# Kernel tuning notes

Hardware: AMD Instinct MI355X
Metric: run time of the kernel (lower is better)

Reference implementation:

```python
import jax, jax.numpy as jnp
import numpy as np

N_USERS = 100_000
N_ITEMS = 50_000
N = N_USERS + N_ITEMS  # total nodes in the normalized UI adjacency
D = 128                # emb_size == hyper_size
NNZ = 1_500_000        # nonzeros in sparse_norm_adj (COO)
EPS = 1e-5             # torch.nn.LayerNorm default eps


def setup_inputs() -> dict:
    key = jax.random.key(0)
    k1, k2, k3, k4 = jax.random.split(key, 4)
    return {
        "ego_embeddings": jax.random.normal(k1, (N, D), dtype=jnp.float32),
        "adj_vals": jax.random.uniform(k2, (NNZ,), dtype=jnp.float32),
        "ln_gamma": jnp.ones((D,), dtype=jnp.float32),
        "ln_beta": jnp.zeros((D,), dtype=jnp.float32),
        "adj_rows": jax.random.randint(k3, (NNZ,), 0, N, dtype=jnp.int32),
        "adj_cols": jax.random.randint(k4, (NNZ,), 0, N, dtype=jnp.int32),
    }


def _layer_norm(x, gamma, beta):
    mu = jnp.mean(x, axis=-1, keepdims=True)
    var = jnp.var(x, axis=-1, keepdims=True)
    return (x - mu) * jax.lax.rsqrt(var + EPS) * gamma + beta


def reference(ego_embeddings, adj_vals, ln_gamma, ln_beta, adj_rows, adj_cols):
    # HGCNConv with act=False: adj @ (adj.T @ embs), adj sparse COO [N, N]
    # (A^T @ x)[c] = sum_{(r,c) in nnz} vals * x[r]
    h = jax.ops.segment_sum(adj_vals[:, None] * ego_embeddings[adj_rows], adj_cols, num_segments=N)
    # (A @ h)[r] = sum_{(r,c) in nnz} vals * h[c]
    h2 = jax.ops.segment_sum(adj_vals[:, None] * h[adj_cols], adj_rows, num_segments=N)
    # LayerNorm + residual (last-layer branch of LocalAwareEncoder.forward)
    out = _layer_norm(h2, ln_gamma, ln_beta) + ego_embeddings
    user_all_embeddings = out[:N_USERS]
    item_all_embeddings = out[N_USERS:]
    return user_all_embeddings, item_all_embeddings
```

## Files before the change

### kernel.cpp

```cpp
#include <hip/hip_runtime.h>

#define N_TOTAL 150000
#define DIM 128
#define NNZ_E 1500000
#define NBUCK 256
#define DPB 586
#define EPB2 2048
#define A2_BLOCKS ((NNZ_E + EPB2 - 1) / EPB2)
#define CONV_BLOCKS 9375
#define HIST_BLOCKS 512
#define MAXE 16
#define G1_BLOCKS (N_TOTAL / 8)
#define SLAB_CAP 8192

typedef unsigned long long u64;
typedef unsigned uvec16 __attribute__((ext_vector_type(16)));
typedef unsigned uvec2  __attribute__((ext_vector_type(2)));

__device__ __forceinline__ unsigned pack_bf16_bits(unsigned ua, unsigned ub) {
    ua = (ua + 0x7FFFu + ((ua >> 16) & 1u)) >> 16;
    ub = (ub + 0x7FFFu + ((ub >> 16) & 1u)) >> 16;
    return ua | (ub << 16);
}
__device__ __forceinline__ unsigned pack_bf16(float a, float b) {
    return pack_bf16_bits(__float_as_uint(a), __float_as_uint(b));
}
__device__ __forceinline__ float2 unpack_bf16(unsigned u) {
    return make_float2(__uint_as_float(u << 16), __uint_as_float(u & 0xFFFF0000u));
}
__device__ __forceinline__ float rdlane_f(float x, int l) {
    return __uint_as_float((unsigned)__builtin_amdgcn_readlane((int)__float_as_uint(x), l));
}

__device__ __forceinline__ int wave_iscan(int v, int lane) {
    #pragma unroll
    for (int o = 1; o < 64; o <<= 1) {
        int u = __shfl_up(v, o, 64);
        if (lane >= o) v += u;
    }
    return v;
}
__device__ __forceinline__ int blk_escan512(int v, int t, int* wsum) {
    int lane = t & 63, wv = t >> 6;
    int inc = wave_iscan(v, lane);
    if (lane == 63) wsum[wv] = inc;
    __syncthreads();
    if (t < 64) {
        int x = (t < 8) ? wsum[t] : 0;
        int p = wave_iscan(x, t);
        if (t < 8) wsum[t] = p - x;
    }
    __syncthreads();
    return wsum[wv] + inc - v;
}

__device__ __forceinline__ void sload_pair(uvec16 &a, uvec16 &b, const void* p) {
    asm volatile("s_load_dwordx16 %0, %2, 0x0\n\t"
                 "s_load_dwordx16 %1, %2, 0x40\n\t"
                 "s_waitcnt lgkmcnt(0)"
                 : "=&s"(a), "=&s"(b) : "s"(p) : "memory");
}
__device__ __forceinline__ void sload_be(uvec2 &r, const void* p) {
    asm volatile("s_load_dwordx2 %0, %1, 0x0\n\t"
                 "s_waitcnt lgkmcnt(0)"
                 : "=&s"(r) : "s"(p) : "memory");
}

__device__ __forceinline__ void chunk8(const uvec16 &m, int lim, int lane,
                                       const uint* __restrict__ srcBf,
                                       float &ax, float &ay, float &bx, float &by) {
    #pragma unroll
    for (int j = 0; j < 8; j++) {
        unsigned sx = (j < lim) ? (m[2 * j] & 0x3FFFFu) : 0u;
        float vv = (j < lim) ? __uint_as_float(m[2 * j + 1]) : 0.0f;
        const uint* p = srcBf + ((size_t)sx << 6);
        float2 uu = unpack_bf16(p[lane]);
        if (j & 1) { bx += vv * uu.x; by += vv * uu.y; }
        else       { ax += vv * uu.x; ay += vv * uu.y; }
    }
}

__device__ __forceinline__ void gather_row(const uint* __restrict__ srcBf,
                                           const int* __restrict__ offs,
                                           const uint2* __restrict__ edges,
                                           int row_u, int lane,
                                           float &ax, float &ay, float &bx, float &by) {
    uvec2 be;
    sload_be(be, offs + row_u);
    int beg = (int)be[0];
    int n = (int)be[1] - beg;
    const u64* ep = (const u64*)edges + beg;
    uvec16 mA, mB;
    sload_pair(mA, mB, ep);
    chunk8(mA, n < 8 ? n : 8, lane, srcBf, ax, ay, bx, by);
    if (n > 8) {
        chunk8(mB, n - 8 < 8 ? n - 8 : 8, lane, srcBf, ax, ay, bx, by);
        if (n > 16) {
            uvec16 mC, mD;
            sload_pair(mC, mD, ep + 16);
            chunk8(mC, n - 16 < 8 ? n - 16 : 8, lane, srcBf, ax, ay, bx, by);
            if (n > 24) {
                chunk8(mD, n - 24 < 8 ? n - 24 : 8, lane, srcBf, ax, ay, bx, by);
                for (int k = 32; k < n; k++) {
                    uint2 e = edges[beg + k];
                    float v = __uint_as_float(e.y);
                    float2 u = unpack_bf16(srcBf[(((size_t)e.x) << 6) + lane]);
                    ax += v * u.x; ay += v * u.y;
                }
            }
        }
    }
}

__global__ __launch_bounds__(256) void conv_hist(const float* __restrict__ in,
                                                 uint* __restrict__ outp,
                                                 const int* __restrict__ rows,
                                                 const int* __restrict__ cols,
                                                 int* __restrict__ cnt1,
                                                 int* __restrict__ cnt2) {
    __shared__ int h[512];
    int t = threadIdx.x;
    if (blockIdx.x < CONV_BLOCKS) {
        int i = blockIdx.x * 256 + t;
        const u64* in8 = (const u64*)in;
        u64 w0 = __builtin_nontemporal_load(&in8[4 * i + 0]);
        u64 w1 = __builtin_nontemporal_load(&in8[4 * i + 1]);
        u64 w2 = __builtin_nontemporal_load(&in8[4 * i + 2]);
        u64 w3 = __builtin_nontemporal_load(&in8[4 * i + 3]);
        uint4 o;
        o.x = pack_bf16_bits((unsigned)w0, (unsigned)(w0 >> 32));
        o.y = pack_bf16_bits((unsigned)w1, (unsigned)(w1 >> 32));
        o.z = pack_bf16_bits((unsigned)w2, (unsigned)(w2 >> 32));
        o.w = pack_bf16_bits((unsigned)w3, (unsigned)(w3 >> 32));
        ((uint4*)outp)[i] = o;
    } else {
        h[t] = 0; h[t + 256] = 0;
        __syncthreads();
        int bid = blockIdx.x - CONV_BLOCKS;
        int stride = HIST_BLOCKS * 256;
        for (int e = bid * 256 + t; e < NNZ_E; e += stride) {
            atomicAdd(&h[cols[e] / DPB], 1);
            atomicAdd(&h[256 + rows[e] / DPB], 1);
        }
        __syncthreads();
        if (h[t]) atomicAdd(&cnt1[t], h[t]);
        if (h[t + 256]) atomicAdd(&cnt2[t], h[t + 256]);
    }
}

__global__ __launch_bounds__(512) void phaseA_fused(const int* __restrict__ rows,
                                                    const int* __restrict__ cols,
                                                    const float* __restrict__ vals,
                                                    const int* __restrict__ gcnt,
                                                    int* __restrict__ gCur,
                                                    int* __restrict__ sbG,
                                                    uint2* __restrict__ slab) {
    __shared__ uint2 sortedL[2 * EPB2];
    __shared__ unsigned short bktL[2 * EPB2];
    __shared__ int cnt[512], off[512], gbase[512];
    __shared__ int part[512];
    __shared__ int wsum[8];
    __shared__ int totE;
    int t = threadIdx.x;
    int base = blockIdx.x * EPB2;
    cnt[t] = 0;

    if (blockIdx.x == 0) {
        int g = gcnt[t];
        part[t] = g; __syncthreads();
        for (int o = 1; o < 256; o <<= 1) {
            int a = ((t & 255) >= o) ? part[t - o] : 0; __syncthreads();
            part[t] += a; __syncthreads();
        }
        sbG[t] = ((t < 256) ? 0 : NNZ_E) + part[t] - g;
        if (t == 0) sbG[512] = 2 * NNZ_E;
    }
    __syncthreads();

    uint2 eA[4], eB[4];
    int rA[4], rB[4];
    short bA[4], bB[4];
    #pragma unroll
    for (int j = 0; j < 4; j++) {
        int e = base + j * 512 + t;
        if (e < NNZ_E) {
            int r = rows[e], c = cols[e];
            unsigned v = __float_as_uint(vals[e]);
            int b1 = c / DPB, dl1 = c - b1 * DPB;
            int b2 = r / DPB, dl2 = r - b2 * DPB;
            bA[j] = (short)b1;
            eA[j].x = ((unsigned)dl1 << 18) | (unsigned)r;
            eA[j].y = v;
            bB[j] = (short)(256 + b2);
            eB[j].x = ((unsigned)dl2 << 18) | (unsigned)c;
            eB[j].y = v;
            rA[j] = atomicAdd(&cnt[b1], 1);
            rB[j] = atomicAdd(&cnt[256 + b2], 1);
        } else { bA[j] = -1; bB[j] = -1; }
    }
    __syncthreads();
    int c0 = cnt[t];
    int bs = blk_escan512(c0, t, wsum);
    off[t] = bs;
    if (t == 511) totE = bs + c0;
    __syncthreads();
    #pragma unroll
    for (int j = 0; j < 4; j++) {
        if (bA[j] >= 0) {
            int p = off[(int)bA[j]] + rA[j];
            sortedL[p] = eA[j]; bktL[p] = (unsigned short)bA[j];
            p = off[(int)bB[j]] + rB[j];
            sortedL[p] = eB[j]; bktL[p] = (unsigned short)bB[j];
        }
    }
    __syncthreads();
    if (cnt[t] > 0) gbase[t] = atomicAdd(&gCur[t], cnt[t]);
    __syncthreads();
    int nE = totE;
    for (int i = t; i < nE; i += 512) {
        int b = bktL[i];
        slab[((size_t)b << 13) + gbase[b] + (i - off[b])] = sortedL[i];
    }
}

__global__ __launch_bounds__(512) void phaseB1(const uint2* __restrict__ slab,
                                               const int* __restrict__ gcnt,
                                               const int* __restrict__ sbG,
                                               int* __restrict__ offs1,
                                               uint2* __restrict__ sorted) {
    __shared__ int cnt[DPB], sc[DPB], cur[DPB], wsum[8];
    int b = blockIdx.x, t = threadIdx.x;
    int n = gcnt[b];
    const uint2* sl = slab + ((size_t)b << 13);
    int sb = sbG[b];
    for (int d = t; d < DPB; d += 512) cnt[d] = 0;
    __syncthreads();
    bool fast = (n <= 512 * MAXE);
    uint2 ent[MAXE]; int rk[MAXE];
    if (fast) {
        #pragma unroll
        for (int k = 0; k < MAXE; k++) {
            int i = t + k * 512;
            bool valid = i < n;
            uint2 e = valid ? sl[i] : make_uint2(0u, 0u);
            ent[k] = e;
            rk[k] = valid ? atomicAdd(&cnt[e.x >> 18], 1) : 0;
        }
    } else {
        for (int i = t; i < n; i += 512)
            atomicAdd(&cnt[sl[i].x >> 18], 1);
    }
    __syncthreads();
    int d0 = 2 * t;
    int c0 = (d0     < DPB) ? cnt[d0]     : 0;
    int c1 = (d0 + 1 < DPB) ? cnt[d0 + 1] : 0;
    int bs = blk_escan512(c0 + c1, t, wsum);
    if (d0     < DPB) { sc[d0]     = bs;      cur[d0]     = bs; }
    if (d0 + 1 < DPB) { sc[d0 + 1] = bs + c0; cur[d0 + 1] = bs + c0; }
    __syncthreads();
    int destBase = b * DPB;
    for (int d = t; d < DPB; d += 512) {
        int dd = destBase + d;
        if (dd <= N_TOTAL) offs1[dd] = sb + sc[d];
    }
    if (fast) {
        #pragma unroll
        for (int k = 0; k < MAXE; k++) {
            int i = t + k * 512;
            if (i < n) {
                int dl = ent[k].x >> 18;
                sorted[sb + sc[dl] + rk[k]] = make_uint2(ent[k].x & 0x3FFFF, ent[k].y);
            }
        }
    } else {
        for (int i = t; i < n; i += 512) {
            uint2 e = sl[i];
            int dl = e.x >> 18;
            int p = atomicAdd(&cur[dl], 1);
            sorted[sb + p] = make_uint2(e.x & 0x3FFFF, e.y);
        }
    }
}

__global__ __launch_bounds__(512) void phaseB2_gather1(const uint2* __restrict__ slab,
                                                       const int* __restrict__ gcnt,
                                                       const int* __restrict__ sbG,
                                                       int* __restrict__ offs2,
                                                       uint2* __restrict__ sorted,
                                                       const uint* __restrict__ egoBf,
                                                       const int* __restrict__ offs1,
                                                       uint* __restrict__ hBf) {
    __shared__ int cnt[DPB], sc[DPB], cur[DPB], wsum[8];
    int t = threadIdx.x;
    if (blockIdx.x < NBUCK) {
        int b = blockIdx.x + NBUCK;
        int n = gcnt[b];
        const uint2* sl = slab + ((size_t)b << 13);
        int sb = sbG[b];
        for (int d = t; d < DPB; d += 512) cnt[d] = 0;
        __syncthreads();
        for (int i = t; i < n; i += 512)
            atomicAdd(&cnt[sl[i].x >> 18], 1);
        __syncthreads();
        int d0 = 2 * t;
        int c0 = (d0     < DPB) ? cnt[d0]     : 0;
        int c1 = (d0 + 1 < DPB) ? cnt[d0 + 1] : 0;
        int bs = blk_escan512(c0 + c1, t, wsum);
        if (d0     < DPB) { sc[d0]     = bs;      cur[d0]     = bs; }
        if (d0 + 1 < DPB) { sc[d0 + 1] = bs + c0; cur[d0 + 1] = bs + c0; }
        __syncthreads();
        int destBase = blockIdx.x * DPB;
        for (int d = t; d < DPB; d += 512) {
            int dd = destBase + d;
            if (dd <= N_TOTAL) offs2[dd] = sb + sc[d];
        }
        for (int i = t; i < n; i += 512) {
            uint2 e = sl[i];
            int dl = e.x >> 18;
            int p = atomicAdd(&cur[dl], 1);
            sorted[sb + p] = make_uint2(e.x & 0x3FFFF, e.y);
        }
    } else {
        int lane = t & 63;
        int row = (blockIdx.x - NBUCK) * 8 + (t >> 6);
        int row_u = __builtin_amdgcn_readfirstlane(row);
        float ax = 0.f, ay = 0.f, bx = 0.f, by = 0.f;
        gather_row(egoBf, offs1, sorted, row_u, lane, ax, ay, bx, by);
        hBf[(size_t)row_u * 64 + lane] = pack_bf16(ax + bx, ay + by);
    }
}

__global__ __launch_bounds__(256) void gather2_ln(const uint* __restrict__ hBf,
                                                  const int* __restrict__ offs,
                                                  const uint2* __restrict__ edges,
                                                  const uint* __restrict__ egoBf,
                                                  const float* __restrict__ gamma,
                                                  const float* __restrict__ beta,
                                                  float* __restrict__ out) {
    int lane = threadIdx.x & 63;
    int row = blockIdx.x * 4 + (threadIdx.x >> 6);
    int row_u = __builtin_amdgcn_readfirstlane(row);
    float ax = 0.f, ay = 0.f, bx = 0.f, by = 0.f;
    gather_row(hBf, offs, edges, row_u, lane, ax, ay, bx, by);
    float2 acc = make_float2(ax + bx, ay + by);
    float s = acc.x + acc.y;
    float sq = acc.x * acc.x + acc.y * acc.y;
    #pragma unroll
    for (int o = 1; o <= 16; o <<= 1) {
        s  += __shfl_xor(s, o, 64);
        sq += __shfl_xor(sq, o, 64);
    }
    float sT  = rdlane_f(s, 0)  + rdlane_f(s, 32);
    float sqT = rdlane_f(sq, 0) + rdlane_f(sq, 32);
    float mu = sT * (1.0f / DIM);
    float var = sqT * (1.0f / DIM) - mu * mu;
    float rs = rsqrtf(var + 1e-5f);
    float2 g  = ((const float2*)gamma)[lane];
    float2 bb = ((const float2*)beta)[lane];
    unsigned egoW = __builtin_nontemporal_load(&egoBf[(size_t)row_u * 64 + lane]);
    float2 e2 = unpack_bf16(egoW);
    float2 o2;
    o2.x = (acc.x - mu) * rs * g.x + bb.x + e2.x;
    o2.y = (acc.y - mu) * rs * g.y + bb.y + e2.y;
    u64 ow = (u64)__float_as_uint(o2.x) | ((u64)__float_as_uint(o2.y) << 32);
    __builtin_nontemporal_store(ow, (u64*)out + (size_t)row_u * 64 + lane);
}

__device__ __forceinline__ void atomic_add_f32(float* p, float v) {
    __hip_atomic_fetch_add(p, v, __ATOMIC_RELAXED, __HIP_MEMORY_SCOPE_AGENT);
}
__global__ void scatter_kernel(const float* __restrict__ src, const float* __restrict__ vals,
                               const int* __restrict__ gidx, const int* __restrict__ sidx,
                               float* __restrict__ dst, int nnz) {
    int gid = blockIdx.x * blockDim.x + threadIdx.x;
    int e = gid >> 5, lane = gid & 31;
    if (e >= nnz) return;
    float v = vals[e];
    float4 x = ((const float4*)(src + (size_t)gidx[e] * DIM))[lane];
    float* d = dst + (size_t)sidx[e] * DIM + lane * 4;
    atomic_add_f32(d + 0, v * x.x); atomic_add_f32(d + 1, v * x.y);
    atomic_add_f32(d + 2, v * x.z); atomic_add_f32(d + 3, v * x.w);
}
__global__ void ln_residual_kernel(const float* __restrict__ h2, const float* __restrict__ ego,
                                   const float* __restrict__ gamma, const float* __restrict__ beta,
                                   float* __restrict__ out, int nrows) {
    int gid = blockIdx.x * blockDim.x + threadIdx.x;
    int row = gid >> 6, lane = gid & 63;
    if (row >= nrows) return;
    float2 x = ((const float2*)(h2 + (size_t)row * DIM))[lane];
    float s = x.x + x.y, sq = x.x * x.x + x.y * x.y;
    #pragma unroll
    for (int o = 32; o > 0; o >>= 1) { s += __shfl_xor(s, o, 64); sq += __shfl_xor(sq, o, 64); }
    float mu = s * (1.0f / DIM), var = sq * (1.0f / DIM) - mu * mu;
    float rs = rsqrtf(var + 1e-5f);
    float2 eg = ((const float2*)(ego + (size_t)row * DIM))[lane];
    float2 g = ((const float2*)gamma)[lane], b = ((const float2*)beta)[lane];
    float2 o2;
    o2.x = (x.x - mu) * rs * g.x + b.x + eg.x;
    o2.y = (x.y - mu) * rs * g.y + b.y + eg.y;
    ((float2*)(out + (size_t)row * DIM))[lane] = o2;
}

extern "C" void kernel_launch(void* const* d_in, const int* in_sizes, int n_in,
                              void* d_out, int out_size, void* d_ws, size_t ws_size,
                              hipStream_t stream) {
    const float* ego   = (const float*)d_in[0];
    const float* vals  = (const float*)d_in[1];
    const float* gamma = (const float*)d_in[2];
    const float* beta  = (const float*)d_in[3];
    const int*   rows  = (const int*)d_in[4];
    const int*   cols  = (const int*)d_in[5];
    float* out = (float*)d_out;

    const size_t EGO_BF_B = (size_t)N_TOTAL * DIM * 2;
    const size_t H_BF_B   = (size_t)N_TOTAL * DIM * 2;
    const size_t SORT_B   = (size_t)2 * NNZ_E * sizeof(uint2);
    const size_t OFFS_B   = ((size_t)N_TOTAL + 16) * sizeof(int);
    const size_t SMALL    = 16384;
    const size_t REQ = EGO_BF_B + H_BF_B + SORT_B + 2 * OFFS_B + SMALL;
    const size_t H_FP32_B = (size_t)N_TOTAL * DIM * sizeof(float);

    char* w = (char*)d_ws;
    uint* egoBf   = (uint*)w;   w += EGO_BF_B;
    uint* hBf     = (uint*)w;   w += H_BF_B;
    uint2* sorted = (uint2*)w;  w += SORT_B;
    int* offs1    = (int*)w;    w += OFFS_B;
    int* offs2    = (int*)w;    w += OFFS_B;
    int* cntArr   = (int*)w;    w += 512 * sizeof(int);
    int* gc       = (int*)w;    w += 512 * sizeof(int);
    int* sb       = (int*)w;    w += 516 * sizeof(int);
    uint2* slab   = (uint2*)d_out;

    if (ws_size >= REQ) {
        (void)hipMemsetAsync(cntArr, 0, 1024 * sizeof(int), stream);
        conv_hist<<<CONV_BLOCKS + HIST_BLOCKS, 256, 0, stream>>>(ego, egoBf, rows, cols,
                                                                 cntArr, cntArr + 256);
        phaseA_fused<<<A2_BLOCKS, 512, 0, stream>>>(rows, cols, vals, cntArr, gc, sb, slab);
        phaseB1<<<NBUCK, 512, 0, stream>>>(slab, cntArr, sb, offs1, sorted);
        phaseB2_gather1<<<NBUCK + G1_BLOCKS, 512, 0, stream>>>(slab, cntArr, sb, offs2,
                                                               sorted, egoBf, offs1, hBf);
        gather2_ln<<<N_TOTAL / 4, 256, 0, stream>>>(hBf, offs2, sorted, egoBf,
                                                    gamma, beta, out);
    } else {
        float* h = (float*)d_ws;
        (void)hipMemsetAsync(h, 0, H_FP32_B, stream);
        (void)hipMemsetAsync(out, 0, H_FP32_B, stream);
        long total = (long)NNZ_E * 32;
        int grid = (int)((total + 255) / 256);
        scatter_kernel<<<grid, 256, 0, stream>>>(ego, vals, rows, cols, h, NNZ_E);
        scatter_kernel<<<grid, 256, 0, stream>>>(h, vals, cols, rows, out, NNZ_E);
        int lngrid = (N_TOTAL * 64 + 255) / 256;
        ln_residual_kernel<<<lngrid, 256, 0, stream>>>(out, ego, gamma, beta, out, N_TOTAL);
    }
}
```

Baseline: 333.9 us.

## Merge histogram, conversion and bucketing into one kernel; fuse both bucket-sort phases

The bf16 conversion, the bucket histogram and the phase-A slab bucketing now run as independent block ranges of one launch. The global prefix over bucket counts is recomputed in every phase-B block, so the sbG array and its serial scan in block 0 go away. Both bucket sets are then sorted by a single 512-block phaseB launch, and gather1 becomes its own kernel. This cuts one launch and lets the row and column sorts run concurrently. In exchange, the gather no longer overlaps with the second sort, and the redundant scans add a little work per block.

```diff
diff --git a/kernel.cpp b/kernel.cpp
--- a/kernel.cpp
+++ b/kernel.cpp
@@ -6,11 +6,10 @@
 #define NBUCK 256
 #define DPB 586
 #define EPB2 2048
-#define A2_BLOCKS ((NNZ_E + EPB2 - 1) / EPB2)
-#define CONV_BLOCKS 9375
-#define HIST_BLOCKS 512
+#define NB_A ((NNZ_E + EPB2 - 1) / EPB2)
+#define NB_H 256
+#define NB_C 4688
 #define MAXE 16
-#define G1_BLOCKS (N_TOTAL / 8)
 #define SLAB_CAP 8192
 
 typedef unsigned long long u64;
@@ -112,127 +111,110 @@
     }
 }
 
-__global__ __launch_bounds__(256) void conv_hist(const float* __restrict__ in,
-                                                 uint* __restrict__ outp,
-                                                 const int* __restrict__ rows,
-                                                 const int* __restrict__ cols,
-                                                 int* __restrict__ cnt1,
-                                                 int* __restrict__ cnt2) {
-    __shared__ int h[512];
-    int t = threadIdx.x;
-    if (blockIdx.x < CONV_BLOCKS) {
-        int i = blockIdx.x * 256 + t;
-        const u64* in8 = (const u64*)in;
-        u64 w0 = __builtin_nontemporal_load(&in8[4 * i + 0]);
-        u64 w1 = __builtin_nontemporal_load(&in8[4 * i + 1]);
-        u64 w2 = __builtin_nontemporal_load(&in8[4 * i + 2]);
-        u64 w3 = __builtin_nontemporal_load(&in8[4 * i + 3]);
-        uint4 o;
-        o.x = pack_bf16_bits((unsigned)w0, (unsigned)(w0 >> 32));
-        o.y = pack_bf16_bits((unsigned)w1, (unsigned)(w1 >> 32));
-        o.z = pack_bf16_bits((unsigned)w2, (unsigned)(w2 >> 32));
-        o.w = pack_bf16_bits((unsigned)w3, (unsigned)(w3 >> 32));
-        ((uint4*)outp)[i] = o;
-    } else {
-        h[t] = 0; h[t + 256] = 0;
-        __syncthreads();
-        int bid = blockIdx.x - CONV_BLOCKS;
-        int stride = HIST_BLOCKS * 256;
-        for (int e = bid * 256 + t; e < NNZ_E; e += stride) {
-            atomicAdd(&h[cols[e] / DPB], 1);
-            atomicAdd(&h[256 + rows[e] / DPB], 1);
-        }
-        __syncthreads();
-        if (h[t]) atomicAdd(&cnt1[t], h[t]);
-        if (h[t + 256]) atomicAdd(&cnt2[t], h[t + 256]);
-    }
-}
-
-__global__ __launch_bounds__(512) void phaseA_fused(const int* __restrict__ rows,
-                                                    const int* __restrict__ cols,
-                                                    const float* __restrict__ vals,
-                                                    const int* __restrict__ gcnt,
-                                                    int* __restrict__ gCur,
-                                                    int* __restrict__ sbG,
-                                                    uint2* __restrict__ slab) {
+__global__ __launch_bounds__(512) void mega(const float* __restrict__ in,
+                                            uint* __restrict__ egoBf,
+                                            const int* __restrict__ rows,
+                                            const int* __restrict__ cols,
+                                            const float* __restrict__ vals,
+                                            int* __restrict__ gcnt,
+                                            int* __restrict__ gCur,
+                                            uint2* __restrict__ slab) {
     __shared__ uint2 sortedL[2 * EPB2];
     __shared__ unsigned short bktL[2 * EPB2];
-    __shared__ int cnt[512], off[512], gbase[512];
-    __shared__ int part[512];
-    __shared__ int wsum[8];
+    __shared__ int cntL[512], off[512], gbase[512], wsum[8];
     __shared__ int totE;
     int t = threadIdx.x;
-    int base = blockIdx.x * EPB2;
-    cnt[t] = 0;
-
-    if (blockIdx.x == 0) {
-        int g = gcnt[t];
-        part[t] = g; __syncthreads();
-        for (int o = 1; o < 256; o <<= 1) {
-            int a = ((t & 255) >= o) ? part[t - o] : 0; __syncthreads();
-            part[t] += a; __syncthreads();
-        }
-        sbG[t] = ((t < 256) ? 0 : NNZ_E) + part[t] - g;
-        if (t == 0) sbG[512] = 2 * NNZ_E;
-    }
-    __syncthreads();
-
-    uint2 eA[4], eB[4];
-    int rA[4], rB[4];
-    short bA[4], bB[4];
-    #pragma unroll
-    for (int j = 0; j < 4; j++) {
-        int e = base + j * 512 + t;
-        if (e < NNZ_E) {
-            int r = rows[e], c = cols[e];
-            unsigned v = __float_as_uint(vals[e]);
-            int b1 = c / DPB, dl1 = c - b1 * DPB;
-            int b2 = r / DPB, dl2 = r - b2 * DPB;
-            bA[j] = (short)b1;
-            eA[j].x = ((unsigned)dl1 << 18) | (unsigned)r;
-            eA[j].y = v;
-            bB[j] = (short)(256 + b2);
-            eB[j].x = ((unsigned)dl2 << 18) | (unsigned)c;
-            eB[j].y = v;
-            rA[j] = atomicAdd(&cnt[b1], 1);
-            rB[j] = atomicAdd(&cnt[256 + b2], 1);
-        } else { bA[j] = -1; bB[j] = -1; }
-    }
-    __syncthreads();
-    int c0 = cnt[t];
-    int bs = blk_escan512(c0, t, wsum);
-    off[t] = bs;
-    if (t == 511) totE = bs + c0;
-    __syncthreads();
-    #pragma unroll
-    for (int j = 0; j < 4; j++) {
-        if (bA[j] >= 0) {
-            int p = off[(int)bA[j]] + rA[j];
-            sortedL[p] = eA[j]; bktL[p] = (unsigned short)bA[j];
-            p = off[(int)bB[j]] + rB[j];
-            sortedL[p] = eB[j]; bktL[p] = (unsigned short)bB[j];
-        }
-    }
-    __syncthreads();
-    if (cnt[t] > 0) gbase[t] = atomicAdd(&gCur[t], cnt[t]);
-    __syncthreads();
-    int nE = totE;
-    for (int i = t; i < nE; i += 512) {
-        int b = bktL[i];
-        slab[((size_t)b << 13) + gbase[b] + (i - off[b])] = sortedL[i];
-    }
-}
-
-__global__ __launch_bounds__(512) void phaseB1(const uint2* __restrict__ slab,
-                                               const int* __restrict__ gcnt,
-                                               const int* __restrict__ sbG,
-                                               int* __restrict__ offs1,
-                                               uint2* __restrict__ sorted) {
-    __shared__ int cnt[DPB], sc[DPB], cur[DPB], wsum[8];
+    if (blockIdx.x < NB_A) {
+        int base = blockIdx.x * EPB2;
+        cntL[t] = 0;
+        __syncthreads();
+        uint2 eA[4], eB[4];
+        int rA[4], rB[4];
+        short bA[4], bB[4];
+        #pragma unroll
+        for (int j = 0; j < 4; j++) {
+            int e = base + j * 512 + t;
+            if (e < NNZ_E) {
+                int r = rows[e], c = cols[e];
+                unsigned v = __float_as_uint(vals[e]);
+                int b1 = c / DPB, dl1 = c - b1 * DPB;
+                int b2 = r / DPB, dl2 = r - b2 * DPB;
+                bA[j] = (short)b1;
+                eA[j].x = ((unsigned)dl1 << 18) | (unsigned)r;
+                eA[j].y = v;
+                bB[j] = (short)(256 + b2);
+                eB[j].x = ((unsigned)dl2 << 18) | (unsigned)c;
+                eB[j].y = v;
+                rA[j] = atomicAdd(&cntL[b1], 1);
+                rB[j] = atomicAdd(&cntL[256 + b2], 1);
+            } else { bA[j] = -1; bB[j] = -1; }
+        }
+        __syncthreads();
+        int c0 = cntL[t];
+        int bs = blk_escan512(c0, t, wsum);
+        off[t] = bs;
+        if (t == 511) totE = bs + c0;
+        __syncthreads();
+        #pragma unroll
+        for (int j = 0; j < 4; j++) {
+            if (bA[j] >= 0) {
+                int p = off[(int)bA[j]] + rA[j];
+                sortedL[p] = eA[j]; bktL[p] = (unsigned short)bA[j];
+                p = off[(int)bB[j]] + rB[j];
+                sortedL[p] = eB[j]; bktL[p] = (unsigned short)bB[j];
+            }
+        }
+        __syncthreads();
+        if (cntL[t] > 0) gbase[t] = atomicAdd(&gCur[t], cntL[t]);
+        __syncthreads();
+        int nE = totE;
+        for (int i = t; i < nE; i += 512) {
+            int b = bktL[i];
+            slab[((size_t)b << 13) + gbase[b] + (i - off[b])] = sortedL[i];
+        }
+    } else if (blockIdx.x < NB_A + NB_H) {
+        cntL[t] = 0;
+        __syncthreads();
+        int bid = blockIdx.x - NB_A;
+        int stride = NB_H * 512;
+        for (int e = bid * 512 + t; e < NNZ_E; e += stride) {
+            atomicAdd(&cntL[cols[e] / DPB], 1);
+            atomicAdd(&cntL[256 + rows[e] / DPB], 1);
+        }
+        __syncthreads();
+        if (cntL[t]) atomicAdd(&gcnt[t], cntL[t]);
+    } else {
+        int i = (blockIdx.x - NB_A - NB_H) * 512 + t;
+        if (i < N_TOTAL * DIM / 8) {
+            const u64* in8 = (const u64*)in;
+            u64 w0 = __builtin_nontemporal_load(&in8[4 * i + 0]);
+            u64 w1 = __builtin_nontemporal_load(&in8[4 * i + 1]);
+            u64 w2 = __builtin_nontemporal_load(&in8[4 * i + 2]);
+            u64 w3 = __builtin_nontemporal_load(&in8[4 * i + 3]);
+            uint4 o;
+            o.x = pack_bf16_bits((unsigned)w0, (unsigned)(w0 >> 32));
+            o.y = pack_bf16_bits((unsigned)w1, (unsigned)(w1 >> 32));
+            o.z = pack_bf16_bits((unsigned)w2, (unsigned)(w2 >> 32));
+            o.w = pack_bf16_bits((unsigned)w3, (unsigned)(w3 >> 32));
+            ((uint4*)egoBf)[i] = o;
+        }
+    }
+}
+
+__global__ __launch_bounds__(512) void phaseB(const uint2* __restrict__ slab,
+                                              const int* __restrict__ gcnt,
+                                              int* __restrict__ offs1,
+                                              int* __restrict__ offs2,
+                                              uint2* __restrict__ sorted) {
+    __shared__ int cnt[DPB], sc[DPB], cur[DPB], part[512], wsum[8];
     int b = blockIdx.x, t = threadIdx.x;
+    int g = gcnt[t];
+    int pre = blk_escan512(g, t, wsum);
+    part[t] = pre;
+    __syncthreads();
+    int sb = part[b];
     int n = gcnt[b];
     const uint2* sl = slab + ((size_t)b << 13);
-    int sb = sbG[b];
     for (int d = t; d < DPB; d += 512) cnt[d] = 0;
     __syncthreads();
     bool fast = (n <= 512 * MAXE);
@@ -258,10 +240,11 @@
     if (d0     < DPB) { sc[d0]     = bs;      cur[d0]     = bs; }
     if (d0 + 1 < DPB) { sc[d0 + 1] = bs + c0; cur[d0 + 1] = bs + c0; }
     __syncthreads();
-    int destBase = b * DPB;
+    int destBase = (b & 255) * DPB;
+    int* offs = (b < NBUCK) ? offs1 : offs2;
     for (int d = t; d < DPB; d += 512) {
         int dd = destBase + d;
-        if (dd <= N_TOTAL) offs1[dd] = sb + sc[d];
+        if (dd <= N_TOTAL) offs[dd] = sb + sc[d];
     }
     if (fast) {
         #pragma unroll
@@ -282,52 +265,16 @@
     }
 }
 
-__global__ __launch_bounds__(512) void phaseB2_gather1(const uint2* __restrict__ slab,
-                                                       const int* __restrict__ gcnt,
-                                                       const int* __restrict__ sbG,
-                                                       int* __restrict__ offs2,
-                                                       uint2* __restrict__ sorted,
-                                                       const uint* __restrict__ egoBf,
-                                                       const int* __restrict__ offs1,
-                                                       uint* __restrict__ hBf) {
-    __shared__ int cnt[DPB], sc[DPB], cur[DPB], wsum[8];
-    int t = threadIdx.x;
-    if (blockIdx.x < NBUCK) {
-        int b = blockIdx.x + NBUCK;
-        int n = gcnt[b];
-        const uint2* sl = slab + ((size_t)b << 13);
-        int sb = sbG[b];
-        for (int d = t; d < DPB; d += 512) cnt[d] = 0;
-        __syncthreads();
-        for (int i = t; i < n; i += 512)
-            atomicAdd(&cnt[sl[i].x >> 18], 1);
-        __syncthreads();
-        int d0 = 2 * t;
-        int c0 = (d0     < DPB) ? cnt[d0]     : 0;
-        int c1 = (d0 + 1 < DPB) ? cnt[d0 + 1] : 0;
-        int bs = blk_escan512(c0 + c1, t, wsum);
-        if (d0     < DPB) { sc[d0]     = bs;      cur[d0]     = bs; }
-        if (d0 + 1 < DPB) { sc[d0 + 1] = bs + c0; cur[d0 + 1] = bs + c0; }
-        __syncthreads();
-        int destBase = blockIdx.x * DPB;
-        for (int d = t; d < DPB; d += 512) {
-            int dd = destBase + d;
-            if (dd <= N_TOTAL) offs2[dd] = sb + sc[d];
-        }
-        for (int i = t; i < n; i += 512) {
-            uint2 e = sl[i];
-            int dl = e.x >> 18;
-            int p = atomicAdd(&cur[dl], 1);
-            sorted[sb + p] = make_uint2(e.x & 0x3FFFF, e.y);
-        }
-    } else {
-        int lane = t & 63;
-        int row = (blockIdx.x - NBUCK) * 8 + (t >> 6);
-        int row_u = __builtin_amdgcn_readfirstlane(row);
-        float ax = 0.f, ay = 0.f, bx = 0.f, by = 0.f;
-        gather_row(egoBf, offs1, sorted, row_u, lane, ax, ay, bx, by);
-        hBf[(size_t)row_u * 64 + lane] = pack_bf16(ax + bx, ay + by);
-    }
+__global__ __launch_bounds__(512) void gather1(const uint* __restrict__ srcBf,
+                                               const int* __restrict__ offs,
+                                               const uint2* __restrict__ edges,
+                                               uint* __restrict__ dstBf) {
+    int lane = threadIdx.x & 63;
+    int row = blockIdx.x * 8 + (threadIdx.x >> 6);
+    int row_u = __builtin_amdgcn_readfirstlane(row);
+    float ax = 0.f, ay = 0.f, bx = 0.f, by = 0.f;
+    gather_row(srcBf, offs, edges, row_u, lane, ax, ay, bx, by);
+    dstBf[(size_t)row_u * 64 + lane] = pack_bf16(ax + bx, ay + by);
 }
 
 __global__ __launch_bounds__(256) void gather2_ln(const uint* __restrict__ hBf,
@@ -428,17 +375,14 @@
     int* offs2    = (int*)w;    w += OFFS_B;
     int* cntArr   = (int*)w;    w += 512 * sizeof(int);
     int* gc       = (int*)w;    w += 512 * sizeof(int);
-    int* sb       = (int*)w;    w += 516 * sizeof(int);
     uint2* slab   = (uint2*)d_out;
 
     if (ws_size >= REQ) {
         (void)hipMemsetAsync(cntArr, 0, 1024 * sizeof(int), stream);
-        conv_hist<<<CONV_BLOCKS + HIST_BLOCKS, 256, 0, stream>>>(ego, egoBf, rows, cols,
-                                                                 cntArr, cntArr + 256);
-        phaseA_fused<<<A2_BLOCKS, 512, 0, stream>>>(rows, cols, vals, cntArr, gc, sb, slab);
-        phaseB1<<<NBUCK, 512, 0, stream>>>(slab, cntArr, sb, offs1, sorted);
-        phaseB2_gather1<<<NBUCK + G1_BLOCKS, 512, 0, stream>>>(slab, cntArr, sb, offs2,
-                                                               sorted, egoBf, offs1, hBf);
+        mega<<<NB_A + NB_H + NB_C, 512, 0, stream>>>(ego, egoBf, rows, cols, vals,
+                                                     cntArr, gc, slab);
+        phaseB<<<512, 512, 0, stream>>>(slab, cntArr, offs1, offs2, sorted);
+        gather1<<<N_TOTAL / 8, 512, 0, stream>>>(egoBf, offs1, sorted, hBf);
         gather2_ln<<<N_TOTAL / 4, 256, 0, stream>>>(hBf, offs2, sorted, egoBf,
                                                     gamma, beta, out);
     } else {
```

New measurement: 323.9 us. 3.0% less time.
